# Kernel optimization log

Hardware: AMD Instinct MI355X
Metric: run time of the kernel (lower is better)

Reference implementation:

```python
import jax, jax.numpy as jnp
import numpy as np

N = 1048576   # total nodes across batch
B = 128       # number of graphs
H = 128       # hidden_size
NEG_SLOPE = 0.01  # LeakyReLU default


def setup_inputs() -> dict:
    key = jax.random.key(0)
    k1, k2, k3, k4 = jax.random.split(key, 4)
    h = jax.random.normal(k1, (N, H), dtype=jnp.float32)
    attention_query = jax.random.normal(k2, (B, H), dtype=jnp.float32)
    w = jax.random.normal(k3, (2 * H,), dtype=jnp.float32) * (1.0 / np.sqrt(2 * H))
    segment_ids = jnp.sort(jax.random.randint(k4, (N,), 0, B, dtype=jnp.int32))
    return {"h": h, "attention_query": attention_query, "w": w, "segment_ids": segment_ids}


def reference(h, attention_query, w, segment_ids):
    # gate_nn(concat([h, q_rep])) = h @ w[:H] + q[seg] @ w[H:], then LeakyReLU
    w_h, w_q = w[:H], w[H:]
    q_score = attention_query @ w_q                      # [B]
    gate = h @ w_h + q_score[segment_ids]                # [N]
    gate = jnp.where(gate >= 0, gate, NEG_SLOPE * gate)  # LeakyReLU
    # segment softmax over nodes of each graph
    m = jax.ops.segment_max(gate, segment_ids, num_segments=B)   # [B]
    m = jnp.where(jnp.isfinite(m), m, 0.0)               # guard empty segments
    e = jnp.exp(gate - m[segment_ids])                   # [N]
    denom = jax.ops.segment_sum(e, segment_ids, num_segments=B)  # [B]
    alpha = e / jnp.maximum(denom, 1e-20)[segment_ids]   # [N]
    # feat_nn takes first half of concat => just h; weighted segment sum
    pooled = jax.ops.segment_sum(alpha[:, None] * h, segment_ids, num_segments=B)  # [B, H]
    return pooled
```

## Files before the change

kernel.cpp:

```cpp
#include <hip/hip_runtime.h>
#include <math.h>

#define N_ROWS 1048576
#define H 128
#define B 128
#define NEG_SLOPE 0.01f

#define GRID_MAIN 4096
#define ROWS_PB (N_ROWS / GRID_MAIN)
#define MAXP 256

__device__ __forceinline__ float dot4(float4 a, float4 b) {
    return a.x * b.x + a.y * b.y + a.z * b.z + a.w * b.w;
}

typedef float v4f __attribute__((ext_vector_type(4)));
__device__ __forceinline__ float4 ldnt(const float4* p) {
    v4f t = __builtin_nontemporal_load((const v4f*)p);
    return make_float4(t.x, t.y, t.z, t.w);
}

__global__ __launch_bounds__(256) void qs_init_kernel(const float* __restrict__ aq,
                                                      const float* __restrict__ w,
                                                      float* __restrict__ qs,
                                                      int* __restrict__ counter) {
    if (blockIdx.x == 0 && threadIdx.x < B) counter[threadIdx.x] = 0;
    const int lane = threadIdx.x & 63;
    const int wave = threadIdx.x >> 6;
    const int half = lane >> 5;
    const int hl   = lane & 31;
    const int b    = blockIdx.x * 8 + wave * 2 + half;
    float4 w4 = ((const float4*)(w + H))[hl];
    float4 a4 = ((const float4*)(aq + (long)b * H))[hl];
    float d = dot4(a4, w4);
    #pragma unroll
    for (int off = 1; off < 32; off <<= 1) d += __shfl_xor(d, off, 32);
    if (hl == 0) qs[b] = d;
}

__global__ __launch_bounds__(256) void main_kernel(const float* __restrict__ h,
                                                   const int* __restrict__ seg,
                                                   const float* __restrict__ w,
                                                   const float* __restrict__ qs,
                                                   int* __restrict__ counter,
                                                   float* __restrict__ pm,
                                                   float* __restrict__ pd,
                                                   float* __restrict__ pacc) {
    __shared__ float qs_s[B];
    __shared__ float sm[4];
    __shared__ float sd[4];
    __shared__ float sacc[4][H];
    if (threadIdx.x < B) qs_s[threadIdx.x] = qs[threadIdx.x];
    __syncthreads();

    const int lane = threadIdx.x & 63;
    const int wave = threadIdx.x >> 6;
    const int half = lane >> 5;
    const int hl   = lane & 31;
    const int hwid = wave * 2 + half;
    const long r0  = (long)blockIdx.x * ROWS_PB;

    float4 w4 = ((const float4*)w)[hl];

    const int sFirst = seg[r0];
    const int sLast  = seg[r0 + ROWS_PB - 1];

    if (sFirst == sLast) {
        const float qsv = qs_s[sFirst];
        float  m_run = -1e30f;
        float  d_run = 0.0f;
        float4 acc   = {0.0f, 0.0f, 0.0f, 0.0f};

        const int NIT = ROWS_PB / 32;
        const float4* hp = (const float4*)(h + (r0 + (long)hwid * 4) * H) + hl;
        float4 h0 = ldnt(hp);
        float4 h1 = ldnt(hp + 32);
        float4 h2 = ldnt(hp + 64);
        float4 h3 = ldnt(hp + 96);

        for (int it = 0; it < NIT; ++it) {
            const bool more = (it + 1 < NIT);
            float4 n0, n1, n2, n3;
            if (more) {
                const float4* np = hp + 1024;
                n0 = ldnt(np);
                n1 = ldnt(np + 32);
                n2 = ldnt(np + 64);
                n3 = ldnt(np + 96);
                hp = np;
            }

            float d0 = dot4(h0, w4), d1 = dot4(h1, w4);
            float d2 = dot4(h2, w4), d3 = dot4(h3, w4);

            float s0 = d0 + __shfl_xor(d0, 16, 32);
            float s1 = d1 + __shfl_xor(d1, 16, 32);
            float s2 = d2 + __shfl_xor(d2, 16, 32);
            float s3 = d3 + __shfl_xor(d3, 16, 32);
            float z01 = (hl & 16) ? s1 : s0;
            float z23 = (hl & 16) ? s3 : s2;
            float t01 = z01 + __shfl_xor(z01, 8, 32);
            float t23 = z23 + __shfl_xor(z23, 8, 32);
            float zz  = (hl & 8) ? t23 : t01;
            zz += __shfl_xor(zz, 4, 32);
            zz += __shfl_xor(zz, 2, 32);
            zz += __shfl_xor(zz, 1, 32);
            float g0 = __shfl(zz,  0, 32) + qsv;
            float g1 = __shfl(zz, 16, 32) + qsv;
            float g2 = __shfl(zz,  8, 32) + qsv;
            float g3 = __shfl(zz, 24, 32) + qsv;
            g0 = (g0 >= 0.0f) ? g0 : NEG_SLOPE * g0;
            g1 = (g1 >= 0.0f) ? g1 : NEG_SLOPE * g1;
            g2 = (g2 >= 0.0f) ? g2 : NEG_SLOPE * g2;
            g3 = (g3 >= 0.0f) ? g3 : NEG_SLOPE * g3;

            float M  = fmaxf(fmaxf(m_run, g0), fmaxf(fmaxf(g1, g2), g3));
            float sc = __expf(m_run - M);
            float e0 = __expf(g0 - M);
            float e1 = __expf(g1 - M);
            float e2 = __expf(g2 - M);
            float e3 = __expf(g3 - M);
            acc.x = fmaf(acc.x, sc, fmaf(e0, h0.x, e1 * h1.x) + fmaf(e2, h2.x, e3 * h3.x));
            acc.y = fmaf(acc.y, sc, fmaf(e0, h0.y, e1 * h1.y) + fmaf(e2, h2.y, e3 * h3.y));
            acc.z = fmaf(acc.z, sc, fmaf(e0, h0.z, e1 * h1.z) + fmaf(e2, h2.z, e3 * h3.z));
            acc.w = fmaf(acc.w, sc, fmaf(e0, h0.w, e1 * h1.w) + fmaf(e2, h2.w, e3 * h3.w));
            d_run = fmaf(d_run, sc, (e0 + e1) + (e2 + e3));
            m_run = M;

            if (more) { h0 = n0; h1 = n1; h2 = n2; h3 = n3; }
        }
        float m_o = __shfl_xor(m_run, 32);
        float d_o = __shfl_xor(d_run, 32);
        float4 a_o;
        a_o.x = __shfl_xor(acc.x, 32);
        a_o.y = __shfl_xor(acc.y, 32);
        a_o.z = __shfl_xor(acc.z, 32);
        a_o.w = __shfl_xor(acc.w, 32);
        float M  = fmaxf(m_run, m_o);
        float ss = __expf(m_run - M);
        float so = __expf(m_o  - M);
        float4 am;
        am.x = acc.x * ss + a_o.x * so;
        am.y = acc.y * ss + a_o.y * so;
        am.z = acc.z * ss + a_o.z * so;
        am.w = acc.w * ss + a_o.w * so;
        float Dm = d_run * ss + d_o * so;

        if (half == 0) ((float4*)&sacc[wave][0])[hl] = am;
        if (lane == 0) { sm[wave] = M; sd[wave] = Dm; }
        __syncthreads();
        if (wave == 0) {
            float Mb = fmaxf(fmaxf(sm[0], sm[1]), fmaxf(sm[2], sm[3]));
            float e0 = __expf(sm[0] - Mb);
            float e1 = __expf(sm[1] - Mb);
            float e2 = __expf(sm[2] - Mb);
            float e3 = __expf(sm[3] - Mb);
            int c = lane * 2;
            float2 a;
            a.x = fmaf(e0, sacc[0][c],     e1 * sacc[1][c])     + fmaf(e2, sacc[2][c],     e3 * sacc[3][c]);
            a.y = fmaf(e0, sacc[0][c + 1], e1 * sacc[1][c + 1]) + fmaf(e2, sacc[2][c + 1], e3 * sacc[3][c + 1]);
            float Db = fmaf(e0, sd[0], e1 * sd[1]) + fmaf(e2, sd[2], e3 * sd[3]);

            int slot = 0;
            if (lane == 0) slot = atomicAdd(counter + sFirst, 1);
            slot = min(__shfl(slot, 0), MAXP - 1);
            long pbase = (long)sFirst * MAXP + slot;
            ((float2*)(pacc + pbase * H))[lane] = a;
            if (lane == 0) { pm[pbase] = Mb; pd[pbase] = Db; }
        }
    } else {
        int    cur   = -1;
        float  m_run = -1e30f;
        float  d_run = 0.0f;
        float4 acc   = {0.0f, 0.0f, 0.0f, 0.0f};

        for (int it = 0; it < ROWS_PB / 16; ++it) {
            long r1 = r0 + hwid + (long)it * 16;
            long r2 = r1 + 8;
            float4 ha = ldnt(((const float4*)(h + r1 * H)) + hl);
            float4 hb = ldnt(((const float4*)(h + r2 * H)) + hl);
            int s1 = seg[r1];
            int s2 = seg[r2];

            #pragma unroll
            for (int k = 0; k < 2; ++k) {
                float4 h4 = k ? hb : ha;
                int    s  = k ? s2 : s1;
                float d = dot4(h4, w4);
                #pragma unroll
                for (int off = 1; off < 32; off <<= 1) d += __shfl_xor(d, off, 32);
                float g = d + qs_s[s];
                g = (g >= 0.0f) ? g : NEG_SLOPE * g;

                if (s != cur) {
                    if (cur >= 0) {
                        int slot = 0;
                        if (hl == 0) slot = atomicAdd(counter + cur, 1);
                        slot = min(__shfl(slot, 0, 32), MAXP - 1);
                        long pbase = (long)cur * MAXP + slot;
                        ((float4*)(pacc + pbase * H))[hl] = acc;
                        if (hl == 0) { pm[pbase] = m_run; pd[pbase] = d_run; }
                    }
                    cur = s;
                    m_run = -1e30f;
                    d_run = 0.0f;
                    acc = make_float4(0.0f, 0.0f, 0.0f, 0.0f);
                }
                if (g <= m_run) {
                    float e = __expf(g - m_run);
                    acc.x += e * h4.x;
                    acc.y += e * h4.y;
                    acc.z += e * h4.z;
                    acc.w += e * h4.w;
                    d_run += e;
                } else {
                    float sc = __expf(m_run - g);
                    acc.x = acc.x * sc + h4.x;
                    acc.y = acc.y * sc + h4.y;
                    acc.z = acc.z * sc + h4.z;
                    acc.w = acc.w * sc + h4.w;
                    d_run = d_run * sc + 1.0f;
                    m_run = g;
                }
            }
        }
        if (cur >= 0) {
            int slot = 0;
            if (hl == 0) slot = atomicAdd(counter + cur, 1);
            slot = min(__shfl(slot, 0, 32), MAXP - 1);
            long pbase = (long)cur * MAXP + slot;
            ((float4*)(pacc + pbase * H))[hl] = acc;
            if (hl == 0) { pm[pbase] = m_run; pd[pbase] = d_run; }
        }
    }
}

__global__ __launch_bounds__(128) void merge_kernel(const int* __restrict__ counter,
                                                    const float* __restrict__ pm,
                                                    const float* __restrict__ pd,
                                                    const float* __restrict__ pacc,
                                                    float* __restrict__ out) {
    const int s = blockIdx.x;
    const int t = threadIdx.x;
    const int c = min(counter[s], MAXP);
    const long sb = (long)s * MAXP;

    __shared__ float red[2];
    __shared__ float scv[MAXP];

    float lm = -1e30f;
    for (int j = t; j < c; j += 128) lm = fmaxf(lm, pm[sb + j]);
    #pragma unroll
    for (int off = 1; off < 64; off <<= 1) lm = fmaxf(lm, __shfl_xor(lm, off));
    if ((t & 63) == 0) red[t >> 6] = lm;
    __syncthreads();
    float M = fmaxf(red[0], red[1]);
    __syncthreads();

    float ld = 0.0f;
    for (int j = t; j < c; j += 128) {
        float sc = __expf(pm[sb + j] - M);
        scv[j] = sc;
        ld += pd[sb + j] * sc;
    }
    #pragma unroll
    for (int off = 1; off < 64; off <<= 1) ld += __shfl_xor(ld, off);
    if ((t & 63) == 0) red[t >> 6] = ld;
    __syncthreads();
    float D = red[0] + red[1];

    float a = 0.0f;
    #pragma unroll 4
    for (int j = 0; j < c; ++j) a += pacc[(sb + j) * H + t] * scv[j];

    out[s * H + t] = (c > 0) ? a / fmaxf(D, 1e-20f) : 0.0f;
}

extern "C" void kernel_launch(void* const* d_in, const int* in_sizes, int n_in,
                              void* d_out, int out_size, void* d_ws, size_t ws_size,
                              hipStream_t stream) {
    const float* h   = (const float*)d_in[0];
    const float* aq  = (const float*)d_in[1];
    const float* w   = (const float*)d_in[2];
    const int*   seg = (const int*)d_in[3];
    float* out = (float*)d_out;

    float* ws      = (float*)d_ws;
    float* qs      = ws;
    int*   counter = (int*)(ws + B);
    float* pm      = ws + 2 * B;
    float* pd      = ws + 2 * B + B * MAXP;
    float* pacc    = ws + 2 * B + 2 * B * MAXP;

    qs_init_kernel<<<16, 256, 0, stream>>>(aq, w, qs, counter);
    main_kernel<<<GRID_MAIN, 256, 0, stream>>>(h, seg, w, qs, counter, pm, pd, pacc);
    merge_kernel<<<B, 128, 0, stream>>>(counter, pm, pd, pacc, out);
}
```

Measured before the change: 664.4 us.

## Double main grid and add two-segment fast path for boundary blocks

Doubles the number of blocks in the main pass so each block handles half as many rows, which raises the count of in-flight loads and should balance work across CUs better. Blocks that straddle exactly two segments now find the boundary by binary search and run the same pipelined vectorised loop with two sets of online-softmax accumulators, instead of dropping into the slower generic per-row path. The cost is twice as many partial slots per segment for the final combine, and the two-segment path doubles the exp and accumulate work in those blocks.

```diff
diff --git a/kernel.cpp b/kernel.cpp
--- a/kernel.cpp
+++ b/kernel.cpp
@@ -6,7 +6,7 @@
 #define B 128
 #define NEG_SLOPE 0.01f
 
-#define GRID_MAIN 4096
+#define GRID_MAIN 8192
 #define ROWS_PB (N_ROWS / GRID_MAIN)
 #define MAXP 256
 
@@ -47,9 +47,9 @@
                                                    float* __restrict__ pd,
                                                    float* __restrict__ pacc) {
     __shared__ float qs_s[B];
-    __shared__ float sm[4];
-    __shared__ float sd[4];
-    __shared__ float sacc[4][H];
+    __shared__ float sm[4][2];
+    __shared__ float sd[4][2];
+    __shared__ float sacc[4][2][H];
     if (threadIdx.x < B) qs_s[threadIdx.x] = qs[threadIdx.x];
     __syncthreads();
 
@@ -64,6 +64,7 @@
 
     const int sFirst = seg[r0];
     const int sLast  = seg[r0 + ROWS_PB - 1];
+    const int NIT = ROWS_PB / 32;
 
     if (sFirst == sLast) {
         const float qsv = qs_s[sFirst];
@@ -71,7 +72,6 @@
         float  d_run = 0.0f;
         float4 acc   = {0.0f, 0.0f, 0.0f, 0.0f};
 
-        const int NIT = ROWS_PB / 32;
         const float4* hp = (const float4*)(h + (r0 + (long)hwid * 4) * H) + hl;
         float4 h0 = ldnt(hp);
         float4 h1 = ldnt(hp + 32);
@@ -146,20 +146,20 @@
         am.w = acc.w * ss + a_o.w * so;
         float Dm = d_run * ss + d_o * so;
 
-        if (half == 0) ((float4*)&sacc[wave][0])[hl] = am;
-        if (lane == 0) { sm[wave] = M; sd[wave] = Dm; }
+        if (half == 0) ((float4*)&sacc[wave][0][0])[hl] = am;
+        if (lane == 0) { sm[wave][0] = M; sd[wave][0] = Dm; }
         __syncthreads();
         if (wave == 0) {
-            float Mb = fmaxf(fmaxf(sm[0], sm[1]), fmaxf(sm[2], sm[3]));
-            float e0 = __expf(sm[0] - Mb);
-            float e1 = __expf(sm[1] - Mb);
-            float e2 = __expf(sm[2] - Mb);
-            float e3 = __expf(sm[3] - Mb);
+            float Mb = fmaxf(fmaxf(sm[0][0], sm[1][0]), fmaxf(sm[2][0], sm[3][0]));
+            float e0 = __expf(sm[0][0] - Mb);
+            float e1 = __expf(sm[1][0] - Mb);
+            float e2 = __expf(sm[2][0] - Mb);
+            float e3 = __expf(sm[3][0] - Mb);
             int c = lane * 2;
             float2 a;
-            a.x = fmaf(e0, sacc[0][c],     e1 * sacc[1][c])     + fmaf(e2, sacc[2][c],     e3 * sacc[3][c]);
-            a.y = fmaf(e0, sacc[0][c + 1], e1 * sacc[1][c + 1]) + fmaf(e2, sacc[2][c + 1], e3 * sacc[3][c + 1]);
-            float Db = fmaf(e0, sd[0], e1 * sd[1]) + fmaf(e2, sd[2], e3 * sd[3]);
+            a.x = fmaf(e0, sacc[0][0][c],     e1 * sacc[1][0][c])     + fmaf(e2, sacc[2][0][c],     e3 * sacc[3][0][c]);
+            a.y = fmaf(e0, sacc[0][0][c + 1], e1 * sacc[1][0][c + 1]) + fmaf(e2, sacc[2][0][c + 1], e3 * sacc[3][0][c + 1]);
+            float Db = fmaf(e0, sd[0][0], e1 * sd[1][0]) + fmaf(e2, sd[2][0], e3 * sd[3][0]);
 
             int slot = 0;
             if (lane == 0) slot = atomicAdd(counter + sFirst, 1);
@@ -168,7 +168,175 @@
             ((float2*)(pacc + pbase * H))[lane] = a;
             if (lane == 0) { pm[pbase] = Mb; pd[pbase] = Db; }
         }
-    } else {
+        return;
+    }
+
+    int a_ = 0, b_ = ROWS_PB - 1;
+    while (b_ - a_ > 1) { int mid = (a_ + b_) >> 1; if (seg[r0 + mid] == sFirst) a_ = mid; else b_ = mid; }
+    const long kabs = r0 + b_;
+
+    if (seg[kabs] == sLast) {
+        const float qsA = qs_s[sFirst];
+        const float qsB = qs_s[sLast];
+        float  mA = -1e30f, dA = 0.0f;  float4 accA = {0.0f, 0.0f, 0.0f, 0.0f};
+        float  mB = -1e30f, dB = 0.0f;  float4 accB = {0.0f, 0.0f, 0.0f, 0.0f};
+
+        const float4* hp = (const float4*)(h + (r0 + (long)hwid * 4) * H) + hl;
+        float4 h0 = ldnt(hp);
+        float4 h1 = ldnt(hp + 32);
+        float4 h2 = ldnt(hp + 64);
+        float4 h3 = ldnt(hp + 96);
+
+        for (int it = 0; it < NIT; ++it) {
+            const bool more = (it + 1 < NIT);
+            float4 n0, n1, n2, n3;
+            if (more) {
+                const float4* np = hp + 1024;
+                n0 = ldnt(np);
+                n1 = ldnt(np + 32);
+                n2 = ldnt(np + 64);
+                n3 = ldnt(np + 96);
+                hp = np;
+            }
+
+            const long rowb = r0 + (long)it * 32 + hwid * 4;
+
+            float d0 = dot4(h0, w4), d1 = dot4(h1, w4);
+            float d2 = dot4(h2, w4), d3 = dot4(h3, w4);
+
+            float s0 = d0 + __shfl_xor(d0, 16, 32);
+            float s1 = d1 + __shfl_xor(d1, 16, 32);
+            float s2 = d2 + __shfl_xor(d2, 16, 32);
+            float s3 = d3 + __shfl_xor(d3, 16, 32);
+            float z01 = (hl & 16) ? s1 : s0;
+            float z23 = (hl & 16) ? s3 : s2;
+            float t01 = z01 + __shfl_xor(z01, 8, 32);
+            float t23 = z23 + __shfl_xor(z23, 8, 32);
+            float zz  = (hl & 8) ? t23 : t01;
+            zz += __shfl_xor(zz, 4, 32);
+            zz += __shfl_xor(zz, 2, 32);
+            zz += __shfl_xor(zz, 1, 32);
+
+            const bool v0 = (rowb + 0) < kabs;
+            const bool v1 = (rowb + 1) < kabs;
+            const bool v2 = (rowb + 2) < kabs;
+            const bool v3 = (rowb + 3) < kabs;
+            float g0 = __shfl(zz,  0, 32) + (v0 ? qsA : qsB);
+            float g1 = __shfl(zz, 16, 32) + (v1 ? qsA : qsB);
+            float g2 = __shfl(zz,  8, 32) + (v2 ? qsA : qsB);
+            float g3 = __shfl(zz, 24, 32) + (v3 ? qsA : qsB);
+            g0 = (g0 >= 0.0f) ? g0 : NEG_SLOPE * g0;
+            g1 = (g1 >= 0.0f) ? g1 : NEG_SLOPE * g1;
+            g2 = (g2 >= 0.0f) ? g2 : NEG_SLOPE * g2;
+            g3 = (g3 >= 0.0f) ? g3 : NEG_SLOPE * g3;
+
+            {
+                float M  = fmaxf(fmaxf(mA, v0 ? g0 : -1e30f),
+                                 fmaxf(fmaxf(v1 ? g1 : -1e30f, v2 ? g2 : -1e30f), v3 ? g3 : -1e30f));
+                float sc = __expf(mA - M);
+                float e0 = v0 ? __expf(g0 - M) : 0.0f;
+                float e1 = v1 ? __expf(g1 - M) : 0.0f;
+                float e2 = v2 ? __expf(g2 - M) : 0.0f;
+                float e3 = v3 ? __expf(g3 - M) : 0.0f;
+                accA.x = fmaf(accA.x, sc, fmaf(e0, h0.x, e1 * h1.x) + fmaf(e2, h2.x, e3 * h3.x));
+                accA.y = fmaf(accA.y, sc, fmaf(e0, h0.y, e1 * h1.y) + fmaf(e2, h2.y, e3 * h3.y));
+                accA.z = fmaf(accA.z, sc, fmaf(e0, h0.z, e1 * h1.z) + fmaf(e2, h2.z, e3 * h3.z));
+                accA.w = fmaf(accA.w, sc, fmaf(e0, h0.w, e1 * h1.w) + fmaf(e2, h2.w, e3 * h3.w));
+                dA = fmaf(dA, sc, (e0 + e1) + (e2 + e3));
+                mA = M;
+            }
+            {
+                float M  = fmaxf(fmaxf(mB, v0 ? -1e30f : g0),
+                                 fmaxf(fmaxf(v1 ? -1e30f : g1, v2 ? -1e30f : g2), v3 ? -1e30f : g3));
+                float sc = __expf(mB - M);
+                float e0 = v0 ? 0.0f : __expf(g0 - M);
+                float e1 = v1 ? 0.0f : __expf(g1 - M);
+                float e2 = v2 ? 0.0f : __expf(g2 - M);
+                float e3 = v3 ? 0.0f : __expf(g3 - M);
+                accB.x = fmaf(accB.x, sc, fmaf(e0, h0.x, e1 * h1.x) + fmaf(e2, h2.x, e3 * h3.x));
+                accB.y = fmaf(accB.y, sc, fmaf(e0, h0.y, e1 * h1.y) + fmaf(e2, h2.y, e3 * h3.y));
+                accB.z = fmaf(accB.z, sc, fmaf(e0, h0.z, e1 * h1.z) + fmaf(e2, h2.z, e3 * h3.z));
+                accB.w = fmaf(accB.w, sc, fmaf(e0, h0.w, e1 * h1.w) + fmaf(e2, h2.w, e3 * h3.w));
+                dB = fmaf(dB, sc, (e0 + e1) + (e2 + e3));
+                mB = M;
+            }
+
+            if (more) { h0 = n0; h1 = n1; h2 = n2; h3 = n3; }
+        }
+
+        float amA_m, amA_d; float4 amA;
+        {
+            float m_o = __shfl_xor(mA, 32);
+            float d_o = __shfl_xor(dA, 32);
+            float4 a_o;
+            a_o.x = __shfl_xor(accA.x, 32);
+            a_o.y = __shfl_xor(accA.y, 32);
+            a_o.z = __shfl_xor(accA.z, 32);
+            a_o.w = __shfl_xor(accA.w, 32);
+            float M  = fmaxf(mA, m_o);
+            float ss = __expf(mA - M);
+            float so = __expf(m_o - M);
+            amA.x = accA.x * ss + a_o.x * so;
+            amA.y = accA.y * ss + a_o.y * so;
+            amA.z = accA.z * ss + a_o.z * so;
+            amA.w = accA.w * ss + a_o.w * so;
+            amA_d = dA * ss + d_o * so;
+            amA_m = M;
+        }
+        float amB_m, amB_d; float4 amB;
+        {
+            float m_o = __shfl_xor(mB, 32);
+            float d_o = __shfl_xor(dB, 32);
+            float4 a_o;
+            a_o.x = __shfl_xor(accB.x, 32);
+            a_o.y = __shfl_xor(accB.y, 32);
+            a_o.z = __shfl_xor(accB.z, 32);
+            a_o.w = __shfl_xor(accB.w, 32);
+            float M  = fmaxf(mB, m_o);
+            float ss = __expf(mB - M);
+            float so = __expf(m_o - M);
+            amB.x = accB.x * ss + a_o.x * so;
+            amB.y = accB.y * ss + a_o.y * so;
+            amB.z = accB.z * ss + a_o.z * so;
+            amB.w = accB.w * ss + a_o.w * so;
+            amB_d = dB * ss + d_o * so;
+            amB_m = M;
+        }
+
+        if (half == 0) {
+            ((float4*)&sacc[wave][0][0])[hl] = amA;
+            ((float4*)&sacc[wave][1][0])[hl] = amB;
+        }
+        if (lane == 0) {
+            sm[wave][0] = amA_m; sd[wave][0] = amA_d;
+            sm[wave][1] = amB_m; sd[wave][1] = amB_d;
+        }
+        __syncthreads();
+        if (wave < 2) {
+            const int sel  = wave;
+            const int sseg = sel ? sLast : sFirst;
+            float Mb = fmaxf(fmaxf(sm[0][sel], sm[1][sel]), fmaxf(sm[2][sel], sm[3][sel]));
+            float e0 = __expf(sm[0][sel] - Mb);
+            float e1 = __expf(sm[1][sel] - Mb);
+            float e2 = __expf(sm[2][sel] - Mb);
+            float e3 = __expf(sm[3][sel] - Mb);
+            int c = lane * 2;
+            float2 a;
+            a.x = fmaf(e0, sacc[0][sel][c],     e1 * sacc[1][sel][c])     + fmaf(e2, sacc[2][sel][c],     e3 * sacc[3][sel][c]);
+            a.y = fmaf(e0, sacc[0][sel][c + 1], e1 * sacc[1][sel][c + 1]) + fmaf(e2, sacc[2][sel][c + 1], e3 * sacc[3][sel][c + 1]);
+            float Db = fmaf(e0, sd[0][sel], e1 * sd[1][sel]) + fmaf(e2, sd[2][sel], e3 * sd[3][sel]);
+
+            int slot = 0;
+            if (lane == 0) slot = atomicAdd(counter + sseg, 1);
+            slot = min(__shfl(slot, 0), MAXP - 1);
+            long pbase = (long)sseg * MAXP + slot;
+            ((float2*)(pacc + pbase * H))[lane] = a;
+            if (lane == 0) { pm[pbase] = Mb; pd[pbase] = Db; }
+        }
+        return;
+    }
+
+    {
         int    cur   = -1;
         float  m_run = -1e30f;
         float  d_run = 0.0f;
```

Measured after the change: 682.3 us. 1.03x slower.
